# Kernel tuning notes

Hardware: AMD Instinct MI355X
Metric: run time of the kernel (lower is better)

## Reference

```python
import jax, jax.numpy as jnp
import numpy as np

B, N, D = 16, 8192, 768
H = int(D * 4.0)  # mlp hidden
EPS = 1e-6
D_SQRT = D ** (-0.5)


def setup_inputs() -> dict:
    key = jax.random.key(0)
    ks = jax.random.split(key, 6)
    x = jax.random.normal(ks[0], (B, N, D), dtype=jnp.float32)
    # learnable query, trunc-normal std = D**-0.5 (plain normal is fine for a reference)
    query = jax.random.normal(ks[1], (D,), dtype=jnp.float32) * D_SQRT
    ln_gamma = jnp.ones((D,), dtype=jnp.float32)
    ln_beta = jnp.zeros((D,), dtype=jnp.float32)
    w1 = jax.random.normal(ks[2], (D, H), dtype=jnp.float32) * (D ** -0.5)
    b1 = jnp.zeros((H,), dtype=jnp.float32)
    w2 = jax.random.normal(ks[3], (H, D), dtype=jnp.float32) * (H ** -0.5)
    b2 = jnp.zeros((D,), dtype=jnp.float32)
    return {"x": x, "query": query, "ln_gamma": ln_gamma, "ln_beta": ln_beta,
            "w1": w1, "b1": b1, "w2": w2, "b2": b2}


def _layernorm(x, gamma, beta):
    mu = jnp.mean(x, axis=-1, keepdims=True)
    var = jnp.mean(jnp.square(x - mu), axis=-1, keepdims=True)
    return (x - mu) * jax.lax.rsqrt(var + EPS) * gamma + beta


def reference(x, query, ln_gamma, ln_beta, w1, b1, w2, b2):
    # single-query cross attention: attn [B, N]
    attn = jnp.einsum('d,bnd->bn', query, x)
    attn_sm = jax.nn.softmax(attn * D_SQRT, axis=-1)
    pooled = jnp.einsum('bn,bnd->bd', attn_sm, x)  # [B, D]
    h = _layernorm(pooled, ln_gamma, ln_beta)
    h = jax.nn.gelu(h @ w1 + b1, approximate=False) @ w2 + b2
    out = pooled + h
    return out, attn
```

## Files before the change

### kernel.cpp

```cpp
#include <hip/hip_runtime.h>
#include <hip/hip_bf16.h>
#include <math.h>

#define BB 16
#define NN 8192
#define DD 768
#define HH 3072
#define EPSV 1e-6f
#define DSQRT 0.03608439182435161f

#define CHUNKS 64
#define ROWS_PER_BLOCK (NN / CHUNKS)
#define NWAVES 4
#define ROWS_PER_WAVE (ROWS_PER_BLOCK / NWAVES)
#define PSTRIDE 772

#define KS1 16
#define KL1 (DD / KS1)
#define KS2 48
#define KL2 (HH / KS2)

__global__ __launch_bounds__(256) void attn_pool_k(
    const float* __restrict__ x, const float* __restrict__ query,
    float* __restrict__ attn_out, float* __restrict__ partials)
{
    const int b     = blockIdx.y;
    const int chunk = blockIdx.x;
    const int tid   = threadIdx.x;
    const int wave  = tid >> 6;
    const int lane  = tid & 63;

    const float4* q4 = (const float4*)query;
    const float4 q0 = q4[lane];
    const float4 q1 = q4[lane + 64];
    const float4 q2 = q4[lane + 128];

    float4 p0 = make_float4(0.f, 0.f, 0.f, 0.f);
    float4 p1 = make_float4(0.f, 0.f, 0.f, 0.f);
    float4 p2 = make_float4(0.f, 0.f, 0.f, 0.f);
    float esum = 0.f;

    const int n0 = chunk * ROWS_PER_BLOCK + wave * ROWS_PER_WAVE;
    const float4* xb = (const float4*)(x + (size_t)b * NN * DD);

    #pragma unroll 2
    for (int r = 0; r < ROWS_PER_WAVE; ++r) {
        const int n = n0 + r;
        const float4* xr = xb + (size_t)n * (DD / 4);
        const float4 v0 = xr[lane];
        const float4 v1 = xr[lane + 64];
        const float4 v2 = xr[lane + 128];

        float s = v0.x * q0.x + v0.y * q0.y + v0.z * q0.z + v0.w * q0.w;
        s += v1.x * q1.x + v1.y * q1.y + v1.z * q1.z + v1.w * q1.w;
        s += v2.x * q2.x + v2.y * q2.y + v2.z * q2.z + v2.w * q2.w;
        #pragma unroll
        for (int off = 32; off > 0; off >>= 1) s += __shfl_xor(s, off);

        if (lane == 0) attn_out[(size_t)b * NN + n] = s;

        const float e = expf(s * DSQRT);
        esum += e;
        p0.x += e * v0.x; p0.y += e * v0.y; p0.z += e * v0.z; p0.w += e * v0.w;
        p1.x += e * v1.x; p1.y += e * v1.y; p1.z += e * v1.z; p1.w += e * v1.w;
        p2.x += e * v2.x; p2.y += e * v2.y; p2.z += e * v2.z; p2.w += e * v2.w;
    }

    __shared__ float lds[NWAVES][PSTRIDE];
    float* my = lds[wave];
    *(float4*)&my[lane * 4]       = p0;
    *(float4*)&my[256 + lane * 4] = p1;
    *(float4*)&my[512 + lane * 4] = p2;
    if (lane == 0) my[768] = esum;
    __syncthreads();

    float* outp = partials + (size_t)(b * CHUNKS + chunk) * PSTRIDE;
    #pragma unroll
    for (int k = 0; k < 3; ++k) {
        const int idx = tid + k * 256;
        outp[idx] = lds[0][idx] + lds[1][idx] + lds[2][idx] + lds[3][idx];
    }
    if (tid == 0) outp[768] = lds[0][768] + lds[1][768] + lds[2][768] + lds[3][768];
}

__global__ __launch_bounds__(256) void reduce_ln_k(
    const float* __restrict__ partials, const float* __restrict__ gamma,
    const float* __restrict__ beta, float* __restrict__ pooled_ws,
    float* __restrict__ hln_ws)
{
    const int b = blockIdx.x, tid = threadIdx.x;
    const float* pb = partials + (size_t)b * CHUNKS * PSTRIDE;

    float v[3];
    #pragma unroll
    for (int k = 0; k < 3; ++k) {
        const int idx = tid + k * 256;
        float s = 0.f;
        #pragma unroll 8
        for (int c = 0; c < CHUNKS; ++c) s += pb[c * PSTRIDE + idx];
        v[k] = s;
    }

    __shared__ float s_den;
    if (tid < 64) {
        float dn = pb[tid * PSTRIDE + 768];
        #pragma unroll
        for (int off = 32; off > 0; off >>= 1) dn += __shfl_xor(dn, off);
        if (tid == 0) s_den = dn;
    }
    __syncthreads();
    const float inv = 1.f / s_den;
    #pragma unroll
    for (int k = 0; k < 3; ++k) v[k] *= inv;

    __shared__ float red[256];
    red[tid] = v[0] + v[1] + v[2];
    __syncthreads();
    for (int s = 128; s > 0; s >>= 1) {
        if (tid < s) red[tid] += red[tid + s];
        __syncthreads();
    }
    const float mu = red[0] * (1.f / 768.f);
    __syncthreads();

    float sq = 0.f;
    #pragma unroll
    for (int k = 0; k < 3; ++k) { const float d = v[k] - mu; sq += d * d; }
    red[tid] = sq;
    __syncthreads();
    for (int s = 128; s > 0; s >>= 1) {
        if (tid < s) red[tid] += red[tid + s];
        __syncthreads();
    }
    const float var = red[0] * (1.f / 768.f);
    const float rstd = rsqrtf(var + EPSV);

    #pragma unroll
    for (int k = 0; k < 3; ++k) {
        const int idx = tid + k * 256;
        pooled_ws[(size_t)b * DD + idx] = v[k];
        hln_ws[(size_t)b * DD + idx] = (v[k] - mu) * rstd * gamma[idx] + beta[idx];
    }
}

__global__ __launch_bounds__(256) void gemm1_part_k(
    const float* __restrict__ hln_ws, const float* __restrict__ w1,
    float* __restrict__ g1p)
{
    const int j  = blockIdx.x * 256 + threadIdx.x;
    const int k0 = blockIdx.y * KL1;

    __shared__ float hl[BB][KL1];
    for (int i = threadIdx.x; i < BB * KL1; i += 256) {
        const int b = i / KL1, d = i - b * KL1;
        hl[b][d] = hln_ws[(size_t)b * DD + k0 + d];
    }
    __syncthreads();

    float wv[KL1];
    #pragma unroll
    for (int d = 0; d < KL1; ++d) wv[d] = w1[(size_t)(k0 + d) * HH + j];

    float acc[BB];
    #pragma unroll
    for (int b = 0; b < BB; ++b) acc[b] = 0.f;

    #pragma unroll
    for (int d4 = 0; d4 < KL1 / 4; ++d4) {
        #pragma unroll
        for (int b = 0; b < BB; ++b) {
            const float4 h4 = *(const float4*)&hl[b][d4 * 4];
            acc[b] += h4.x * wv[d4 * 4] + h4.y * wv[d4 * 4 + 1]
                    + h4.z * wv[d4 * 4 + 2] + h4.w * wv[d4 * 4 + 3];
        }
    }

    float* op = g1p + (size_t)blockIdx.y * BB * HH;
    #pragma unroll
    for (int b = 0; b < BB; ++b) op[(size_t)b * HH + j] = acc[b];
}

__global__ __launch_bounds__(256) void comb1_gelu_k(
    const float* __restrict__ g1p, const float* __restrict__ b1,
    float* __restrict__ h1_ws)
{
    const int i = blockIdx.x * 256 + threadIdx.x;
    const int j = (i * 4) % HH;

    float4 a = *(const float4*)&b1[j];
    #pragma unroll
    for (int s = 0; s < KS1; ++s) {
        const float4 p = *(const float4*)&g1p[(size_t)s * BB * HH + (size_t)i * 4];
        a.x += p.x; a.y += p.y; a.z += p.z; a.w += p.w;
    }
    float4 g;
    g.x = 0.5f * a.x * (1.f + erff(a.x * 0.70710678118654752f));
    g.y = 0.5f * a.y * (1.f + erff(a.y * 0.70710678118654752f));
    g.z = 0.5f * a.z * (1.f + erff(a.z * 0.70710678118654752f));
    g.w = 0.5f * a.w * (1.f + erff(a.w * 0.70710678118654752f));
    *(float4*)&h1_ws[(size_t)i * 4] = g;
}

__global__ __launch_bounds__(256) void gemm2_part_k(
    const float* __restrict__ h1_ws, const float* __restrict__ w2,
    float* __restrict__ g2p)
{
    const int col = blockIdx.x * 256 + threadIdx.x;
    const int k0  = blockIdx.y * KL2;

    __shared__ float hg[BB][KL2];
    for (int i = threadIdx.x; i < BB * KL2; i += 256) {
        const int b = i / KL2, d = i - b * KL2;
        hg[b][d] = h1_ws[(size_t)b * HH + k0 + d];
    }
    __syncthreads();

    float wv[KL2];
    #pragma unroll
    for (int d = 0; d < KL2; ++d) wv[d] = w2[(size_t)(k0 + d) * DD + col];

    float acc[BB];
    #pragma unroll
    for (int b = 0; b < BB; ++b) acc[b] = 0.f;

    #pragma unroll
    for (int d4 = 0; d4 < KL2 / 4; ++d4) {
        #pragma unroll
        for (int b = 0; b < BB; ++b) {
            const float4 h4 = *(const float4*)&hg[b][d4 * 4];
            acc[b] += h4.x * wv[d4 * 4] + h4.y * wv[d4 * 4 + 1]
                    + h4.z * wv[d4 * 4 + 2] + h4.w * wv[d4 * 4 + 3];
        }
    }

    float* op = g2p + (size_t)blockIdx.y * BB * DD;
    #pragma unroll
    for (int b = 0; b < BB; ++b) op[(size_t)b * DD + col] = acc[b];
}

__global__ __launch_bounds__(256) void comb2_fin_k(
    const float* __restrict__ g2p, const float* __restrict__ pooled_ws,
    const float* __restrict__ b2, float* __restrict__ out)
{
    const int i = blockIdx.x * 256 + threadIdx.x;
    const int d = (i * 4) % DD;

    const float4 pl = *(const float4*)&pooled_ws[(size_t)i * 4];
    float4 a = *(const float4*)&b2[d];
    a.x += pl.x; a.y += pl.y; a.z += pl.z; a.w += pl.w;
    #pragma unroll
    for (int s = 0; s < KS2; ++s) {
        const float4 p = *(const float4*)&g2p[(size_t)s * BB * DD + (size_t)i * 4];
        a.x += p.x; a.y += p.y; a.z += p.z; a.w += p.w;
    }
    *(float4*)&out[(size_t)i * 4] = a;
}

extern "C" void kernel_launch(void* const* d_in, const int* in_sizes, int n_in,
                              void* d_out, int out_size, void* d_ws, size_t ws_size,
                              hipStream_t stream)
{
    const float* x     = (const float*)d_in[0];
    const float* query = (const float*)d_in[1];
    const float* gamma = (const float*)d_in[2];
    const float* beta  = (const float*)d_in[3];
    const float* w1    = (const float*)d_in[4];
    const float* b1    = (const float*)d_in[5];
    const float* w2    = (const float*)d_in[6];
    const float* b2    = (const float*)d_in[7];

    float* out      = (float*)d_out;
    float* attn_out = out + BB * DD;

    float* ws       = (float*)d_ws;
    float* partials = ws;
    float* pooled   = partials + BB * CHUNKS * PSTRIDE;
    float* hln      = pooled + BB * DD;
    float* h1       = hln + BB * DD;
    float* g1p      = h1 + BB * HH;
    float* g2p      = g1p + KS1 * BB * HH;

    attn_pool_k<<<dim3(CHUNKS, BB), 256, 0, stream>>>(x, query, attn_out, partials);
    reduce_ln_k<<<dim3(BB), 256, 0, stream>>>(partials, gamma, beta, pooled, hln);
    gemm1_part_k<<<dim3(HH / 256, KS1), 256, 0, stream>>>(hln, w1, g1p);
    comb1_gelu_k<<<dim3(BB * HH / 1024), 256, 0, stream>>>(g1p, b1, h1);
    gemm2_part_k<<<dim3(DD / 256, KS2), 256, 0, stream>>>(h1, w2, g2p);
    comb2_fin_k<<<dim3(BB * DD / 1024), 256, 0, stream>>>(g2p, pooled, b2, out);
}
```

Measured before the change: 116.3 us.

## Fuse post-attention MLP stages into one cooperative kernel with grid syncs

Replaces five separate kernel launches (reduce+layernorm, gemm1 split-K, combine+GELU, gemm2 split-K, final combine) with a single cooperative kernel of 192 blocks separated by grid.sync barriers. The chunk reduction is also split into a two-level reduction so the first phase uses all 192 blocks instead of 16. This targets per-launch overhead and small-grid underutilisation in the latency-bound tail, at the cost of grid-wide barrier overhead and extra workspace traffic.

```diff
diff --git a/kernel.cpp b/kernel.cpp
--- a/kernel.cpp
+++ b/kernel.cpp
@@ -1,6 +1,9 @@
 #include <hip/hip_runtime.h>
+#include <hip/hip_cooperative_groups.h>
 #include <hip/hip_bf16.h>
 #include <math.h>
+
+namespace cg = cooperative_groups;
 
 #define BB 16
 #define NN 8192
@@ -19,6 +22,7 @@
 #define KL1 (DD / KS1)
 #define KS2 48
 #define KL2 (HH / KS2)
+#define CBLK 192
 
 __global__ __launch_bounds__(256) void attn_pool_k(
     const float* __restrict__ x, const float* __restrict__ query,
@@ -83,177 +87,167 @@
     if (tid == 0) outp[768] = lds[0][768] + lds[1][768] + lds[2][768] + lds[3][768];
 }
 
-__global__ __launch_bounds__(256) void reduce_ln_k(
-    const float* __restrict__ partials, const float* __restrict__ gamma,
-    const float* __restrict__ beta, float* __restrict__ pooled_ws,
-    float* __restrict__ hln_ws)
+struct MlpParams {
+    const float* partials;
+    const float* gamma; const float* beta;
+    const float* w1; const float* b1;
+    const float* w2; const float* b2;
+    float* qsum; float* qden;
+    float* pooled; float* hln;
+    float* g1p; float* h1; float* g2p;
+    float* out;
+};
+
+__global__ __launch_bounds__(256) void mlp_coop_k(MlpParams P)
 {
-    const int b = blockIdx.x, tid = threadIdx.x;
-    const float* pb = partials + (size_t)b * CHUNKS * PSTRIDE;
-
-    float v[3];
-    #pragma unroll
-    for (int k = 0; k < 3; ++k) {
-        const int idx = tid + k * 256;
+    cg::grid_group grid = cg::this_grid();
+    const int bid = blockIdx.x;
+    const int tid = threadIdx.x;
+    __shared__ float smem[1024];
+
+    {
+        const int b = bid / 12, r = bid % 12;
+        const int slice = r % 3, q = r / 3;
+        const float* pb = P.partials + (size_t)b * CHUNKS * PSTRIDE;
+        const int col = slice * 256 + tid;
         float s = 0.f;
-        #pragma unroll 8
-        for (int c = 0; c < CHUNKS; ++c) s += pb[c * PSTRIDE + idx];
-        v[k] = s;
-    }
-
-    __shared__ float s_den;
-    if (tid < 64) {
-        float dn = pb[tid * PSTRIDE + 768];
-        #pragma unroll
-        for (int off = 32; off > 0; off >>= 1) dn += __shfl_xor(dn, off);
-        if (tid == 0) s_den = dn;
-    }
-    __syncthreads();
-    const float inv = 1.f / s_den;
-    #pragma unroll
-    for (int k = 0; k < 3; ++k) v[k] *= inv;
-
-    __shared__ float red[256];
-    red[tid] = v[0] + v[1] + v[2];
-    __syncthreads();
-    for (int s = 128; s > 0; s >>= 1) {
-        if (tid < s) red[tid] += red[tid + s];
-        __syncthreads();
-    }
-    const float mu = red[0] * (1.f / 768.f);
-    __syncthreads();
-
-    float sq = 0.f;
-    #pragma unroll
-    for (int k = 0; k < 3; ++k) { const float d = v[k] - mu; sq += d * d; }
-    red[tid] = sq;
-    __syncthreads();
-    for (int s = 128; s > 0; s >>= 1) {
-        if (tid < s) red[tid] += red[tid + s];
-        __syncthreads();
-    }
-    const float var = red[0] * (1.f / 768.f);
-    const float rstd = rsqrtf(var + EPSV);
-
-    #pragma unroll
-    for (int k = 0; k < 3; ++k) {
-        const int idx = tid + k * 256;
-        pooled_ws[(size_t)b * DD + idx] = v[k];
-        hln_ws[(size_t)b * DD + idx] = (v[k] - mu) * rstd * gamma[idx] + beta[idx];
-    }
-}
-
-__global__ __launch_bounds__(256) void gemm1_part_k(
-    const float* __restrict__ hln_ws, const float* __restrict__ w1,
-    float* __restrict__ g1p)
-{
-    const int j  = blockIdx.x * 256 + threadIdx.x;
-    const int k0 = blockIdx.y * KL1;
-
-    __shared__ float hl[BB][KL1];
-    for (int i = threadIdx.x; i < BB * KL1; i += 256) {
-        const int b = i / KL1, d = i - b * KL1;
-        hl[b][d] = hln_ws[(size_t)b * DD + k0 + d];
-    }
-    __syncthreads();
-
-    float wv[KL1];
-    #pragma unroll
-    for (int d = 0; d < KL1; ++d) wv[d] = w1[(size_t)(k0 + d) * HH + j];
-
-    float acc[BB];
-    #pragma unroll
-    for (int b = 0; b < BB; ++b) acc[b] = 0.f;
-
-    #pragma unroll
-    for (int d4 = 0; d4 < KL1 / 4; ++d4) {
-        #pragma unroll
-        for (int b = 0; b < BB; ++b) {
-            const float4 h4 = *(const float4*)&hl[b][d4 * 4];
-            acc[b] += h4.x * wv[d4 * 4] + h4.y * wv[d4 * 4 + 1]
-                    + h4.z * wv[d4 * 4 + 2] + h4.w * wv[d4 * 4 + 3];
-        }
-    }
-
-    float* op = g1p + (size_t)blockIdx.y * BB * HH;
-    #pragma unroll
-    for (int b = 0; b < BB; ++b) op[(size_t)b * HH + j] = acc[b];
-}
-
-__global__ __launch_bounds__(256) void comb1_gelu_k(
-    const float* __restrict__ g1p, const float* __restrict__ b1,
-    float* __restrict__ h1_ws)
-{
-    const int i = blockIdx.x * 256 + threadIdx.x;
-    const int j = (i * 4) % HH;
-
-    float4 a = *(const float4*)&b1[j];
-    #pragma unroll
-    for (int s = 0; s < KS1; ++s) {
-        const float4 p = *(const float4*)&g1p[(size_t)s * BB * HH + (size_t)i * 4];
-        a.x += p.x; a.y += p.y; a.z += p.z; a.w += p.w;
-    }
-    float4 g;
-    g.x = 0.5f * a.x * (1.f + erff(a.x * 0.70710678118654752f));
-    g.y = 0.5f * a.y * (1.f + erff(a.y * 0.70710678118654752f));
-    g.z = 0.5f * a.z * (1.f + erff(a.z * 0.70710678118654752f));
-    g.w = 0.5f * a.w * (1.f + erff(a.w * 0.70710678118654752f));
-    *(float4*)&h1_ws[(size_t)i * 4] = g;
-}
-
-__global__ __launch_bounds__(256) void gemm2_part_k(
-    const float* __restrict__ h1_ws, const float* __restrict__ w2,
-    float* __restrict__ g2p)
-{
-    const int col = blockIdx.x * 256 + threadIdx.x;
-    const int k0  = blockIdx.y * KL2;
-
-    __shared__ float hg[BB][KL2];
-    for (int i = threadIdx.x; i < BB * KL2; i += 256) {
-        const int b = i / KL2, d = i - b * KL2;
-        hg[b][d] = h1_ws[(size_t)b * HH + k0 + d];
-    }
-    __syncthreads();
-
-    float wv[KL2];
-    #pragma unroll
-    for (int d = 0; d < KL2; ++d) wv[d] = w2[(size_t)(k0 + d) * DD + col];
-
-    float acc[BB];
-    #pragma unroll
-    for (int b = 0; b < BB; ++b) acc[b] = 0.f;
-
-    #pragma unroll
-    for (int d4 = 0; d4 < KL2 / 4; ++d4) {
-        #pragma unroll
-        for (int b = 0; b < BB; ++b) {
-            const float4 h4 = *(const float4*)&hg[b][d4 * 4];
-            acc[b] += h4.x * wv[d4 * 4] + h4.y * wv[d4 * 4 + 1]
-                    + h4.z * wv[d4 * 4 + 2] + h4.w * wv[d4 * 4 + 3];
-        }
-    }
-
-    float* op = g2p + (size_t)blockIdx.y * BB * DD;
-    #pragma unroll
-    for (int b = 0; b < BB; ++b) op[(size_t)b * DD + col] = acc[b];
-}
-
-__global__ __launch_bounds__(256) void comb2_fin_k(
-    const float* __restrict__ g2p, const float* __restrict__ pooled_ws,
-    const float* __restrict__ b2, float* __restrict__ out)
-{
-    const int i = blockIdx.x * 256 + threadIdx.x;
-    const int d = (i * 4) % DD;
-
-    const float4 pl = *(const float4*)&pooled_ws[(size_t)i * 4];
-    float4 a = *(const float4*)&b2[d];
-    a.x += pl.x; a.y += pl.y; a.z += pl.z; a.w += pl.w;
-    #pragma unroll
-    for (int s = 0; s < KS2; ++s) {
-        const float4 p = *(const float4*)&g2p[(size_t)s * BB * DD + (size_t)i * 4];
-        a.x += p.x; a.y += p.y; a.z += p.z; a.w += p.w;
-    }
-    *(float4*)&out[(size_t)i * 4] = a;
+        #pragma unroll
+        for (int c = 0; c < CHUNKS / 4; ++c) s += pb[(q * (CHUNKS / 4) + c) * PSTRIDE + col];
+        P.qsum[(size_t)(b * 4 + q) * DD + col] = s;
+        if (slice == 0 && tid == 0) {
+            float dn = 0.f;
+            #pragma unroll
+            for (int c = 0; c < CHUNKS / 4; ++c) dn += pb[(q * (CHUNKS / 4) + c) * PSTRIDE + 768];
+            P.qden[b * 4 + q] = dn;
+        }
+    }
+    grid.sync();
+
+    if (bid < BB) {
+        const int b = bid;
+        float v[3];
+        #pragma unroll
+        for (int k = 0; k < 3; ++k) {
+            const int col = tid + k * 256;
+            float s = 0.f;
+            #pragma unroll
+            for (int q = 0; q < 4; ++q) s += P.qsum[(size_t)(b * 4 + q) * DD + col];
+            v[k] = s;
+        }
+        const float den = P.qden[b * 4] + P.qden[b * 4 + 1]
+                        + P.qden[b * 4 + 2] + P.qden[b * 4 + 3];
+        const float inv = 1.f / den;
+        #pragma unroll
+        for (int k = 0; k < 3; ++k) v[k] *= inv;
+
+        smem[tid] = v[0] + v[1] + v[2];
+        __syncthreads();
+        for (int s = 128; s > 0; s >>= 1) {
+            if (tid < s) smem[tid] += smem[tid + s];
+            __syncthreads();
+        }
+        const float mu = smem[0] * (1.f / 768.f);
+        __syncthreads();
+
+        float sq = 0.f;
+        #pragma unroll
+        for (int k = 0; k < 3; ++k) { const float d = v[k] - mu; sq += d * d; }
+        smem[tid] = sq;
+        __syncthreads();
+        for (int s = 128; s > 0; s >>= 1) {
+            if (tid < s) smem[tid] += smem[tid + s];
+            __syncthreads();
+        }
+        const float rstd = rsqrtf(smem[0] * (1.f / 768.f) + EPSV);
+
+        #pragma unroll
+        for (int k = 0; k < 3; ++k) {
+            const int col = tid + k * 256;
+            P.pooled[(size_t)b * DD + col] = v[k];
+            P.hln[(size_t)b * DD + col] = (v[k] - mu) * rstd * P.gamma[col] + P.beta[col];
+        }
+    }
+    grid.sync();
+
+    {
+        const int jb = bid % 12, ks = bid / 12;
+        const int k0 = ks * KL1;
+        for (int i = tid; i < BB * KL1; i += 256)
+            smem[i] = P.hln[(size_t)(i / KL1) * DD + k0 + (i % KL1)];
+        __syncthreads();
+
+        const int j = jb * 256 + tid;
+        float wv[KL1];
+        #pragma unroll
+        for (int d = 0; d < KL1; ++d) wv[d] = P.w1[(size_t)(k0 + d) * HH + j];
+
+        float acc[BB];
+        #pragma unroll
+        for (int b = 0; b < BB; ++b) acc[b] = 0.f;
+        #pragma unroll
+        for (int d4 = 0; d4 < KL1 / 4; ++d4) {
+            #pragma unroll
+            for (int b = 0; b < BB; ++b) {
+                const float4 h4 = *(const float4*)&smem[b * KL1 + d4 * 4];
+                acc[b] += h4.x * wv[d4 * 4] + h4.y * wv[d4 * 4 + 1]
+                        + h4.z * wv[d4 * 4 + 2] + h4.w * wv[d4 * 4 + 3];
+            }
+        }
+        #pragma unroll
+        for (int b = 0; b < BB; ++b)
+            P.g1p[((size_t)ks * BB + b) * HH + j] = acc[b];
+        __syncthreads();
+    }
+    grid.sync();
+
+    {
+        const int i = bid * 256 + tid;
+        const int j = i % HH;
+        float a = P.b1[j];
+        #pragma unroll
+        for (int s = 0; s < KS1; ++s) a += P.g1p[(size_t)s * BB * HH + i];
+        P.h1[i] = 0.5f * a * (1.f + erff(a * 0.70710678118654752f));
+    }
+    grid.sync();
+
+    if (bid < 144) {
+        const int cb = bid % 3, ks = bid / 3;
+        const int k0 = ks * KL2;
+        for (int i = tid; i < BB * KL2; i += 256)
+            smem[i] = P.h1[(size_t)(i / KL2) * HH + k0 + (i % KL2)];
+        __syncthreads();
+
+        const int col = cb * 256 + tid;
+        float wv[KL2];
+        #pragma unroll
+        for (int d = 0; d < KL2; ++d) wv[d] = P.w2[(size_t)(k0 + d) * DD + col];
+
+        float acc[BB];
+        #pragma unroll
+        for (int b = 0; b < BB; ++b) acc[b] = 0.f;
+        #pragma unroll
+        for (int d4 = 0; d4 < KL2 / 4; ++d4) {
+            #pragma unroll
+            for (int b = 0; b < BB; ++b) {
+                const float4 h4 = *(const float4*)&smem[b * KL2 + d4 * 4];
+                acc[b] += h4.x * wv[d4 * 4] + h4.y * wv[d4 * 4 + 1]
+                        + h4.z * wv[d4 * 4 + 2] + h4.w * wv[d4 * 4 + 3];
+            }
+        }
+        #pragma unroll
+        for (int b = 0; b < BB; ++b)
+            P.g2p[((size_t)ks * BB + b) * DD + col] = acc[b];
+    }
+    grid.sync();
+
+    if (bid < 48) {
+        const int i = bid * 256 + tid;
+        const int d = i % DD;
+        float a = P.pooled[i] + P.b2[d];
+        #pragma unroll
+        for (int s = 0; s < KS2; ++s) a += P.g2p[(size_t)s * BB * DD + i];
+        P.out[i] = a;
+    }
 }
 
 extern "C" void kernel_launch(void* const* d_in, const int* in_sizes, int n_in,
@@ -274,16 +268,22 @@
 
     float* ws       = (float*)d_ws;
     float* partials = ws;
-    float* pooled   = partials + BB * CHUNKS * PSTRIDE;
+    float* qsum     = partials + BB * CHUNKS * PSTRIDE;
+    float* qden     = qsum + BB * 4 * DD;
+    float* pooled   = qden + 64;
     float* hln      = pooled + BB * DD;
     float* h1       = hln + BB * DD;
     float* g1p      = h1 + BB * HH;
     float* g2p      = g1p + KS1 * BB * HH;
 
     attn_pool_k<<<dim3(CHUNKS, BB), 256, 0, stream>>>(x, query, attn_out, partials);
-    reduce_ln_k<<<dim3(BB), 256, 0, stream>>>(partials, gamma, beta, pooled, hln);
-    gemm1_part_k<<<dim3(HH / 256, KS1), 256, 0, stream>>>(hln, w1, g1p);
-    comb1_gelu_k<<<dim3(BB * HH / 1024), 256, 0, stream>>>(g1p, b1, h1);
-    gemm2_part_k<<<dim3(DD / 256, KS2), 256, 0, stream>>>(h1, w2, g2p);
-    comb2_fin_k<<<dim3(BB * DD / 1024), 256, 0, stream>>>(g2p, pooled, b2, out);
+
+    MlpParams p;
+    p.partials = partials; p.gamma = gamma; p.beta = beta;
+    p.w1 = w1; p.b1 = b1; p.w2 = w2; p.b2 = b2;
+    p.qsum = qsum; p.qden = qden; p.pooled = pooled; p.hln = hln;
+    p.g1p = g1p; p.h1 = h1; p.g2p = g2p; p.out = out;
+    void* kargs[] = { (void*)&p };
+    hipLaunchCooperativeKernel((void*)mlp_coop_k, dim3(CBLK), dim3(256),
+                               kargs, 0, stream);
 }
```

Result: slower. 215.6 us (+85.4%).
